# Kernel tuning notes

Measured on AMD Instinct MI355X. Metric: run time of the kernel, lower is better.

## Reference

```python
import jax, jax.numpy as jnp
import numpy as np

N_NODES = 100000
N_EDGES = 600000
D_IN = 128
D_HID = 128
NB_LAYERS = 3
EPS = 1e-5  # torch LayerNorm default


def setup_inputs() -> dict:
    key = jax.random.key(0)
    ks = jax.random.split(key, 12)
    x = jax.random.normal(ks[0], (N_NODES, D_IN), dtype=jnp.float32)
    edge_index = jax.random.randint(ks[1], (2, N_EDGES), 0, N_NODES, dtype=jnp.int32)
    # MLP sizes: [2*D_IN, D_HID, D_HID, D_HID, 1]
    sizes = [2 * D_IN] + [D_HID] * NB_LAYERS + [1]
    inp = {"x": x, "edge_index": edge_index}
    for i in range(len(sizes) - 1):
        scale = 1.0 / np.sqrt(sizes[i]).astype(np.float32)
        inp[f"W{i}"] = jax.random.normal(ks[2 + i], (sizes[i], sizes[i + 1]), dtype=jnp.float32) * scale
        inp[f"b{i}"] = jnp.zeros((sizes[i + 1],), dtype=jnp.float32)
    for i in range(NB_LAYERS):
        inp[f"g{i}"] = jnp.ones((D_HID,), dtype=jnp.float32)      # LayerNorm gamma
        inp[f"beta{i}"] = jnp.zeros((D_HID,), dtype=jnp.float32)  # LayerNorm beta
    return inp


def _layernorm(h, g, b):
    mu = jnp.mean(h, axis=-1, keepdims=True)
    var = jnp.var(h, axis=-1, keepdims=True)
    return (h - mu) * jax.lax.rsqrt(var + EPS) * g + b


def reference(x, edge_index, W0, b0, W1, b1, W2, b2, W3, b3, g0, beta0, g1, beta1, g2, beta2):
    start, end = edge_index[0], edge_index[1]
    # gather node pairs and concat -> [E, 2*D_IN]
    h = jnp.concatenate([x[start], x[end]], axis=1)
    for W, b, g, be in ((W0, b0, g0, beta0), (W1, b1, g1, beta1), (W2, b2, g2, beta2)):
        h = jnp.tanh(_layernorm(h @ W + b, g, be))
    return (h @ W3 + b3).squeeze(-1)  # [E]
```

## Files before the change

### kernel.cpp

```cpp
#include <hip/hip_runtime.h>
#include <hip/hip_bf16.h>


typedef float f32x4 __attribute__((ext_vector_type(4)));
typedef __bf16 bf16x8 __attribute__((ext_vector_type(8)));
typedef unsigned int u32x4 __attribute__((ext_vector_type(4)));

#define MFMA16(a, b, c) __builtin_amdgcn_mfma_f32_16x16x32_bf16((a), (b), (c), 0, 0, 0)
#define TWO_LOG2E 2.885390081777927f

static __device__ __forceinline__ unsigned short bf16bits(float f) {
  __bf16 h = (__bf16)f;
  return __builtin_bit_cast(unsigned short, h);
}

static __device__ __forceinline__ unsigned pack2(float a, float b) {
  return (unsigned)bf16bits(a) | ((unsigned)bf16bits(b) << 16);
}

static __device__ __forceinline__ float tanh_fast2(float z) {
#if __has_builtin(__builtin_amdgcn_exp2f)
  const float ex = __builtin_amdgcn_exp2f(z);
#else
  const float ex = exp2f(z);
#endif
  return 1.0f - 2.0f * __builtin_amdgcn_rcpf(ex + 1.0f);
}

static __device__ __forceinline__ void gload_lds16(const void* g, void* l) {
  __builtin_amdgcn_global_load_lds(
      (const __attribute__((address_space(1))) void*)g,
      (__attribute__((address_space(3))) void*)l, 16, 0, 0);
}

static __device__ __forceinline__ int permk(int k) {
  const int j = k & 7, g = (k >> 3) & 3;
  return (k & ~31) | ((j >> 2) << 4) | (g << 2) | (j & 3);
}

__global__ void prep_x(const float* __restrict__ x,
                       unsigned short* __restrict__ xb, int n8) {
  int gid = blockIdx.x * blockDim.x + threadIdx.x;
  const int stride = gridDim.x * blockDim.x;
  for (int i = gid; i < n8; i += stride) {
    const float4 a = ((const float4*)x)[i * 2];
    const float4 b = ((const float4*)x)[i * 2 + 1];
    u32x4 o;
    o[0] = pack2(a.x, a.y); o[1] = pack2(a.z, a.w);
    o[2] = pack2(b.x, b.y); o[3] = pack2(b.z, b.w);
    ((u32x4*)xb)[i] = o;
  }
}

__global__ void prep_w(const float* __restrict__ W0, const float* __restrict__ W1,
                       const float* __restrict__ W2,
                       const float* __restrict__ B0, const float* __restrict__ G0,
                       const float* __restrict__ Q0,
                       const float* __restrict__ B1, const float* __restrict__ G1,
                       const float* __restrict__ Q1,
                       const float* __restrict__ B2, const float* __restrict__ G2,
                       const float* __restrict__ Q2,
                       const float* __restrict__ W3,
                       unsigned short* __restrict__ wt, float* __restrict__ pp) {
  const int t = blockIdx.x;
  const int tid = threadIdx.x;
  if (t == 8) {
    for (int i = tid; i < 1280; i += 256) {
      const int a = i >> 7, o = i & 127;
      float v;
      switch (a) {
        case 0: v = B0[o]; break;
        case 1: v = G0[o] * TWO_LOG2E; break;
        case 2: v = Q0[o] * TWO_LOG2E; break;
        case 3: v = B1[o]; break;
        case 4: v = G1[o] * TWO_LOG2E; break;
        case 5: v = Q1[o] * TWO_LOG2E; break;
        case 6: v = B2[o]; break;
        case 7: v = G2[o] * TWO_LOG2E; break;
        case 8: v = Q2[o] * TWO_LOG2E; break;
        default: v = W3[o]; break;
      }
      pp[i] = v;
    }
    return;
  }
  const float* src; int kbase; int perm;
  if (t < 4)      { src = W0; kbase = t * 64;      perm = 0; }
  else if (t < 6) { src = W1; kbase = (t - 4) * 64; perm = 1; }
  else            { src = W2; kbase = (t - 6) * 64; perm = 1; }
  char* base = (char*)wt + t * 16384;
  const int col = tid & 127;
  const int kb  = (tid >> 7) << 1;
  #pragma unroll
  for (int i = 0; i < 16; ++i) {
    const int kl = kb + (i << 2);
    const int k0 = kbase + kl;
    const int c0 = perm ? permk(k0) : k0;
    const float wa = src[c0 * 128 + col];
    const float wb = src[(c0 + 1) * 128 + col];
    const unsigned pk = pack2(wa, wb);
    const int off = ((col * 64 + kl) * 2) ^ ((col & 7) << 4);
    *(unsigned*)(base + off) = pk;
  }
}

#define P_B0 0
#define P_G0 128
#define P_Q0 256
#define P_B1 384
#define P_G1 512
#define P_Q1 640
#define P_B2 768
#define P_G2 896
#define P_Q2 1024
#define P_W3 1152

template <int XB>
__global__ __launch_bounds__(256, 3) void edge_mlp(
    const float* __restrict__ x, const int* __restrict__ ei,
    const float* __restrict__ B3,
    const unsigned short* __restrict__ wt, const float* __restrict__ pp,
    const unsigned short* __restrict__ xb,
    float* __restrict__ out, int nE)
{
  __shared__ __align__(16) char lds[32768 + 5120];
  float* plds = (float*)(lds + 32768);
  const int tid  = threadIdx.x;
  const int lane = tid & 63;
  const int wv   = tid >> 6;
  const int e    = lane & 15;
  const int g    = lane >> 4;

  const int wbase = blockIdx.x * 128 + wv * 32;
  const int e0 = wbase + e;
  const int e1 = wbase + 16 + e;
  const int ec0 = e0 < nE ? e0 : nE - 1;
  const int ec1 = e1 < nE ? e1 : nE - 1;
  const int ns0 = ei[ec0], ne0 = ei[nE + ec0];
  const int ns1 = ei[ec1], ne1 = ei[nE + ec1];

  auto stageW = [&](int t, int buf) {
    #pragma unroll
    for (int c = 0; c < 4; ++c) {
      const int o = wv * 4096 + c * 1024;
      gload_lds16((const char*)wt + t * 16384 + o + lane * 16,
                  lds + buf * 16384 + o);
    }
  };

  auto loadW = [&](int buf, int m, int kl) -> bf16x8 {
    const int col = m * 16 + e;
    const int off = ((col * 64 + kl) * 2) ^ ((col & 7) << 4);
    return *(const bf16x8*)(lds + buf * 16384 + off);
  };

  auto loadX = [&](int node, int ko) -> bf16x8 {
    if (XB) {
      return *(const bf16x8*)(xb + (size_t)node * 128 + ko);
    } else {
      const float* src = x + (size_t)node * 128 + ko;
      const float4 ua = *(const float4*)(src);
      const float4 ub = *(const float4*)(src + 4);
      bf16x8 a;
      a[0] = (__bf16)ua.x; a[1] = (__bf16)ua.y; a[2] = (__bf16)ua.z; a[3] = (__bf16)ua.w;
      a[4] = (__bf16)ub.x; a[5] = (__bf16)ub.y; a[6] = (__bf16)ub.z; a[7] = (__bf16)ub.w;
      return a;
    }
  };

  f32x4 acc[8][2];

  auto initAcc = [&](int pb) {
    #pragma unroll
    for (int m = 0; m < 8; ++m) {
      const f32x4 bq = *(const f32x4*)(plds + pb + m * 16 + g * 4);
      acc[m][0] = bq; acc[m][1] = bq;
    }
  };

  auto l0step = [&](int u0, int buf) {
    #pragma unroll
    for (int du = 0; du < 2; ++du) {
      const int u = u0 + du;
      const int ko = (u & 3) * 32 + g * 8;
      const bf16x8 xf0 = loadX(u < 4 ? ns0 : ne0, ko);
      const bf16x8 xf1 = loadX(u < 4 ? ns1 : ne1, ko);
      const int kl = du * 32 + g * 8;
      #pragma unroll
      for (int m = 0; m < 8; ++m) {
        const bf16x8 wf = loadW(buf, m, kl);
        acc[m][0] = MFMA16(wf, xf0, acc[m][0]);
        acc[m][1] = MFMA16(wf, xf1, acc[m][1]);
      }
    }
  };

  unsigned p0[2][8], p1[2][8];

  auto epi = [&](int pg, int pq) {
    #pragma unroll
    for (int j = 0; j < 2; ++j) {
      float s1 = 0.f, s2 = 0.f;
      #pragma unroll
      for (int m = 0; m < 8; ++m)
        #pragma unroll
        for (int r = 0; r < 4; ++r) {
          const float t = acc[m][j][r];
          s1 += t;
          s2 = __builtin_fmaf(t, t, s2);
        }
      s1 += __shfl_xor(s1, 16); s2 += __shfl_xor(s2, 16);
      s1 += __shfl_xor(s1, 32); s2 += __shfl_xor(s2, 32);
      const float mu  = s1 * 0.0078125f;
      const float inv = __builtin_amdgcn_rsqf(s2 * 0.0078125f - mu * mu + 1e-5f);
      const float nm  = -mu * inv;
      #pragma unroll
      for (int m = 0; m < 8; ++m) {
        const f32x4 gq = *(const f32x4*)(plds + pg + m * 16 + g * 4);
        const f32x4 qq = *(const f32x4*)(plds + pq + m * 16 + g * 4);
        float th[4];
        #pragma unroll
        for (int r = 0; r < 4; ++r) {
          const float an = __builtin_fmaf(acc[m][j][r], inv, nm);
          const float z  = __builtin_fmaf(an, gq[r], qq[r]);
          th[r] = tanh_fast2(z);
        }
        p0[j][m] = pack2(th[0], th[1]);
        p1[j][m] = pack2(th[2], th[3]);
      }
    }
  };

  auto lstep = [&](int u0, int buf) {
    #pragma unroll
    for (int du = 0; du < 2; ++du) {
      const int u = u0 + du;
      const int kl = du * 32 + g * 8;
      u32x4 w0, w1;
      w0[0] = p0[0][2 * u];     w0[1] = p1[0][2 * u];
      w0[2] = p0[0][2 * u + 1]; w0[3] = p1[0][2 * u + 1];
      w1[0] = p0[1][2 * u];     w1[1] = p1[1][2 * u];
      w1[2] = p0[1][2 * u + 1]; w1[3] = p1[1][2 * u + 1];
      const bf16x8 bf0 = __builtin_bit_cast(bf16x8, w0);
      const bf16x8 bf1 = __builtin_bit_cast(bf16x8, w1);
      #pragma unroll
      for (int m = 0; m < 8; ++m) {
        const bf16x8 wf = loadW(buf, m, kl);
        acc[m][0] = MFMA16(wf, bf0, acc[m][0]);
        acc[m][1] = MFMA16(wf, bf1, acc[m][1]);
      }
    }
  };

  stageW(0, 0);
  for (int i = tid; i < 1280; i += 256) plds[i] = pp[i];
  __syncthreads();

  initAcc(P_B0);
  stageW(1, 1); l0step(0, 0); __syncthreads();
  stageW(2, 0); l0step(2, 1); __syncthreads();
  stageW(3, 1); l0step(4, 0); __syncthreads();
  stageW(4, 0); l0step(6, 1); __syncthreads();
  stageW(5, 1);
  epi(P_G0, P_Q0); initAcc(P_B1); lstep(0, 0); __syncthreads();
  stageW(6, 0);
  lstep(2, 1); __syncthreads();
  stageW(7, 1);
  epi(P_G1, P_Q1); initAcc(P_B2); lstep(0, 0); __syncthreads();
  lstep(2, 1);

  const float b3v = B3[0];
  #pragma unroll
  for (int j = 0; j < 2; ++j) {
    float s1 = 0.f, s2 = 0.f;
    #pragma unroll
    for (int m = 0; m < 8; ++m)
      #pragma unroll
      for (int r = 0; r < 4; ++r) {
        const float t = acc[m][j][r];
        s1 += t;
        s2 = __builtin_fmaf(t, t, s2);
      }
    s1 += __shfl_xor(s1, 16); s2 += __shfl_xor(s2, 16);
    s1 += __shfl_xor(s1, 32); s2 += __shfl_xor(s2, 32);
    const float mu  = s1 * 0.0078125f;
    const float inv = __builtin_amdgcn_rsqf(s2 * 0.0078125f - mu * mu + 1e-5f);
    const float nm  = -mu * inv;
    float d = 0.f;
    #pragma unroll
    for (int m = 0; m < 8; ++m) {
      const f32x4 gq  = *(const f32x4*)(plds + P_G2 + m * 16 + g * 4);
      const f32x4 qq  = *(const f32x4*)(plds + P_Q2 + m * 16 + g * 4);
      const f32x4 w3q = *(const f32x4*)(plds + P_W3 + m * 16 + g * 4);
      #pragma unroll
      for (int r = 0; r < 4; ++r) {
        const float an = __builtin_fmaf(acc[m][j][r], inv, nm);
        const float z  = __builtin_fmaf(an, gq[r], qq[r]);
        d = __builtin_fmaf(tanh_fast2(z), w3q[r], d);
      }
    }
    d += __shfl_xor(d, 16);
    d += __shfl_xor(d, 32);
    const int eid = wbase + j * 16 + e;
    if (g == 0 && eid < nE) out[eid] = d + b3v;
  }
}

extern "C" void kernel_launch(void* const* d_in, const int* in_sizes, int n_in,
                              void* d_out, int out_size, void* d_ws, size_t ws_size,
                              hipStream_t stream) {
  const float* x  = (const float*)d_in[0];
  const int*   ei = (const int*)d_in[1];
  const float* W0 = (const float*)d_in[2];
  const float* B0 = (const float*)d_in[3];
  const float* W1 = (const float*)d_in[4];
  const float* B1 = (const float*)d_in[5];
  const float* W2 = (const float*)d_in[6];
  const float* B2 = (const float*)d_in[7];
  const float* W3 = (const float*)d_in[8];
  const float* B3 = (const float*)d_in[9];
  const float* G0 = (const float*)d_in[10];
  const float* Q0 = (const float*)d_in[11];
  const float* G1 = (const float*)d_in[12];
  const float* Q1 = (const float*)d_in[13];
  const float* G2 = (const float*)d_in[14];
  const float* Q2 = (const float*)d_in[15];
  float* out = (float*)d_out;

  const int nX = in_sizes[0];
  const int nE = in_sizes[1] / 2;
  const int blocks = (nE + 127) / 128;

  const size_t xb_bytes = ((size_t)nX * 2 + 255) & ~(size_t)255;
  const int use_xb = (ws_size >= xb_bytes + 131072 + 5120) ? 1 : 0;

  unsigned short* xbp = (unsigned short*)d_ws;
  unsigned short* wt  = use_xb ? (unsigned short*)((char*)d_ws + xb_bytes)
                               : (unsigned short*)d_ws;
  float* pp = (float*)((char*)wt + 131072);

  hipLaunchKernelGGL(prep_w, dim3(9), dim3(256), 0, stream,
                     W0, W1, W2, B0, G0, Q0, B1, G1, Q1, B2, G2, Q2, W3, wt, pp);
  if (use_xb) {
    hipLaunchKernelGGL(prep_x, dim3(1024), dim3(256), 0, stream, x, xbp, nX / 8);
    hipLaunchKernelGGL(edge_mlp<1>, dim3(blocks), dim3(256), 0, stream,
                       x, ei, B3, wt, pp, xbp, out, nE);
  } else {
    hipLaunchKernelGGL(edge_mlp<0>, dim3(blocks), dim3(256), 0, stream,
                       x, ei, B3, wt, pp, xbp, out, nE);
  }
}
```

Before: 149.8 us.

## Prefetch gathered node features one slab ahead and split LayerNorm reduction chains

Layer-0 gathers of node features are now issued one K-slab ahead into alternating register buffers, so the random global loads overlap the MFMAs of the previous slab instead of stalling them. The LayerNorm sum and sum-of-squares reductions are split into two independent accumulator chains to shorten the dependent add chain. The cost is extra VGPRs for the prefetch buffers, which could pressure occupancy under launch bounds of 3 waves per SIMD.

New measurement: 150.4 us. No clear change (+0.4%).

```diff
diff --git a/kernel.cpp b/kernel.cpp
--- a/kernel.cpp
+++ b/kernel.cpp
@@ -120,7 +120,7 @@
     const float* __restrict__ x, const int* __restrict__ ei,
     const float* __restrict__ B3,
     const unsigned short* __restrict__ wt, const float* __restrict__ pp,
-    const unsigned short* __restrict__ xb,
+    const unsigned short* __restrict__ xbp,
     float* __restrict__ out, int nE)
 {
   __shared__ __align__(16) char lds[32768 + 5120];
@@ -156,7 +156,7 @@
 
   auto loadX = [&](int node, int ko) -> bf16x8 {
     if (XB) {
-      return *(const bf16x8*)(xb + (size_t)node * 128 + ko);
+      return *(const bf16x8*)(xbp + (size_t)node * 128 + ko);
     } else {
       const float* src = x + (size_t)node * 128 + ko;
       const float4 ua = *(const float4*)(src);
@@ -168,6 +168,16 @@
     }
   };
 
+  auto ldslab = [&](int u0, bf16x8* dst) {
+    #pragma unroll
+    for (int du = 0; du < 2; ++du) {
+      const int u = u0 + du;
+      const int ko = (u & 3) * 32 + g * 8;
+      dst[du * 2 + 0] = loadX(u < 4 ? ns0 : ne0, ko);
+      dst[du * 2 + 1] = loadX(u < 4 ? ns1 : ne1, ko);
+    }
+  };
+
   f32x4 acc[8][2];
 
   auto initAcc = [&](int pb) {
@@ -178,19 +188,15 @@
     }
   };
 
-  auto l0step = [&](int u0, int buf) {
+  auto l0mfma = [&](const bf16x8* xf, int buf) {
     #pragma unroll
     for (int du = 0; du < 2; ++du) {
-      const int u = u0 + du;
-      const int ko = (u & 3) * 32 + g * 8;
-      const bf16x8 xf0 = loadX(u < 4 ? ns0 : ne0, ko);
-      const bf16x8 xf1 = loadX(u < 4 ? ns1 : ne1, ko);
       const int kl = du * 32 + g * 8;
       #pragma unroll
       for (int m = 0; m < 8; ++m) {
         const bf16x8 wf = loadW(buf, m, kl);
-        acc[m][0] = MFMA16(wf, xf0, acc[m][0]);
-        acc[m][1] = MFMA16(wf, xf1, acc[m][1]);
+        acc[m][0] = MFMA16(wf, xf[du * 2 + 0], acc[m][0]);
+        acc[m][1] = MFMA16(wf, xf[du * 2 + 1], acc[m][1]);
       }
     }
   };
@@ -200,15 +206,19 @@
   auto epi = [&](int pg, int pq) {
     #pragma unroll
     for (int j = 0; j < 2; ++j) {
-      float s1 = 0.f, s2 = 0.f;
-      #pragma unroll
-      for (int m = 0; m < 8; ++m)
+      float s1a = 0.f, s1b = 0.f, s2a = 0.f, s2b = 0.f;
+      #pragma unroll
+      for (int m = 0; m < 8; m += 2) {
         #pragma unroll
         for (int r = 0; r < 4; ++r) {
-          const float t = acc[m][j][r];
-          s1 += t;
-          s2 = __builtin_fmaf(t, t, s2);
+          const float ta = acc[m][j][r];
+          const float tb = acc[m + 1][j][r];
+          s1a += ta; s1b += tb;
+          s2a = __builtin_fmaf(ta, ta, s2a);
+          s2b = __builtin_fmaf(tb, tb, s2b);
         }
+      }
+      float s1 = s1a + s1b, s2 = s2a + s2b;
       s1 += __shfl_xor(s1, 16); s2 += __shfl_xor(s2, 16);
       s1 += __shfl_xor(s1, 32); s2 += __shfl_xor(s2, 32);
       const float mu  = s1 * 0.0078125f;
@@ -252,15 +262,17 @@
     }
   };
 
+  bf16x8 xra[4], xrb[4];
   stageW(0, 0);
   for (int i = tid; i < 1280; i += 256) plds[i] = pp[i];
+  ldslab(0, xra);
   __syncthreads();
 
   initAcc(P_B0);
-  stageW(1, 1); l0step(0, 0); __syncthreads();
-  stageW(2, 0); l0step(2, 1); __syncthreads();
-  stageW(3, 1); l0step(4, 0); __syncthreads();
-  stageW(4, 0); l0step(6, 1); __syncthreads();
+  stageW(1, 1); ldslab(2, xrb); l0mfma(xra, 0); __syncthreads();
+  stageW(2, 0); ldslab(4, xra); l0mfma(xrb, 1); __syncthreads();
+  stageW(3, 1); ldslab(6, xrb); l0mfma(xra, 0); __syncthreads();
+  stageW(4, 0); l0mfma(xrb, 1); __syncthreads();
   stageW(5, 1);
   epi(P_G0, P_Q0); initAcc(P_B1); lstep(0, 0); __syncthreads();
   stageW(6, 0);
@@ -272,15 +284,19 @@
   const float b3v = B3[0];
   #pragma unroll
   for (int j = 0; j < 2; ++j) {
-    float s1 = 0.f, s2 = 0.f;
-    #pragma unroll
-    for (int m = 0; m < 8; ++m)
+    float s1a = 0.f, s1b = 0.f, s2a = 0.f, s2b = 0.f;
+    #pragma unroll
+    for (int m = 0; m < 8; m += 2) {
       #pragma unroll
       for (int r = 0; r < 4; ++r) {
-        const float t = acc[m][j][r];
-        s1 += t;
-        s2 = __builtin_fmaf(t, t, s2);
-      }
+        const float ta = acc[m][j][r];
+        const float tb = acc[m + 1][j][r];
+        s1a += ta; s1b += tb;
+        s2a = __builtin_fmaf(ta, ta, s2a);
+        s2b = __builtin_fmaf(tb, tb, s2b);
+      }
+    }
+    float s1 = s1a + s1b, s2 = s2a + s2b;
     s1 += __shfl_xor(s1, 16); s2 += __shfl_xor(s2, 16);
     s1 += __shfl_xor(s1, 32); s2 += __shfl_xor(s2, 32);
     const float mu  = s1 * 0.0078125f;
```
